# Kernel tuning notes

Hardware: AMD Instinct MI355X
Metric: run time of the kernel (lower is better)

## Reference

```python
import jax, jax.numpy as jnp
import numpy as np

N_USERS = 200000
N_ITEMS = 100000
N_NODES = N_USERS + N_ITEMS
EMBED_DIM = 64
N_LAYERS = 3
N_EDGES = 5000000
BATCH = 4096


def setup_inputs() -> dict:
    key = jax.random.key(0)
    ks = jax.random.split(key, 8)
    # Xavier-uniform-ish init for embedding tables
    lim = float(np.sqrt(6.0 / (N_USERS + EMBED_DIM)))
    user_emb = jax.random.uniform(ks[0], (N_USERS, EMBED_DIM), jnp.float32, -lim, lim)
    lim_i = float(np.sqrt(6.0 / (N_ITEMS + EMBED_DIM)))
    item_emb = jax.random.uniform(ks[1], (N_ITEMS, EMBED_DIM), jnp.float32, -lim_i, lim_i)
    # sparse normalized adjacency in COO form (values ~ 1/sqrt(du*di), use small positives)
    adj_vals = jax.random.uniform(ks[2], (N_EDGES,), jnp.float32, 0.0, 0.1)
    adj_rows = jax.random.randint(ks[3], (N_EDGES,), 0, N_NODES, jnp.int32)
    adj_cols = jax.random.randint(ks[4], (N_EDGES,), 0, N_NODES, jnp.int32)
    users = jax.random.randint(ks[5], (BATCH,), 0, N_USERS, jnp.int32)
    pos_items = jax.random.randint(ks[6], (BATCH,), 0, N_ITEMS, jnp.int32)
    neg_items = jax.random.randint(ks[7], (BATCH,), 0, N_ITEMS, jnp.int32)
    return {
        "user_emb": user_emb, "item_emb": item_emb, "adj_vals": adj_vals,
        "adj_rows": adj_rows, "adj_cols": adj_cols,
        "users": users, "pos_items": pos_items, "neg_items": neg_items,
    }


def _spmm(adj_rows, adj_cols, adj_vals, x):
    # y = A @ x for sparse COO A: gather source rows, scale, scatter-add to dest rows
    msgs = adj_vals[:, None] * x[adj_cols]          # [n_edges, d]
    return jax.ops.segment_sum(msgs, adj_rows, num_segments=N_NODES)


def reference(user_emb, item_emb, adj_vals, adj_rows, adj_cols, users, pos_items, neg_items):
    # E^0 = concat(user, item); E^k = A @ E^{k-1}; final = mean over k=0..K
    E = jnp.concatenate([user_emb, item_emb], axis=0)   # [N_NODES, d]
    acc = E
    cur = E
    for _ in range(N_LAYERS):
        cur = _spmm(adj_rows, adj_cols, adj_vals, cur)
        acc = acc + cur
    E_final = acc / jnp.asarray(N_LAYERS + 1, E.dtype)
    e_u = E_final[users]                         # users index into user block
    e_pos = E_final[N_USERS + pos_items]         # items offset by n_users
    e_neg = E_final[N_USERS + neg_items]
    return jnp.stack([e_u, e_pos, e_neg], axis=0)  # [3, B, d]
```

## Files before the change

kernel.cpp:

```cpp
#include <hip/hip_runtime.h>
#include <hip/hip_fp16.h>
#include <stdint.h>

#define N_USERS   200000
#define N_ITEMS   100000
#define N_NODES   300000
#define EMBED_DIM 64
#define N_EDGES   5000000
#define BATCH     4096

#define ROWS_PER_BUCKET 512
#define PART_K 586
#define PART_B 1024
#define CHUNK  4884
#define PART_L (PART_K * PART_B)
#define SCAN_T 1024
#define SCAN_NB (PART_L / SCAN_T)

#define VAL_SCALE 81920.0f
#define VAL_INV   (1.0f / 81920.0f)
#define FIN_CAP   10240

__device__ __forceinline__ int swz(int b)     { return ((b & 7) << 7) | (b >> 3); }

__global__ void part_count(const int* __restrict__ rows, int* __restrict__ hist) {
    __shared__ int h[PART_K];
    for (int i = threadIdx.x; i < PART_K; i += blockDim.x) h[i] = 0;
    __syncthreads();
    int beg = blockIdx.x * CHUNK;
    int end = min(beg + CHUNK, N_EDGES);
    for (int i = beg + (int)threadIdx.x * 4; i < end; i += blockDim.x * 4) {
        int4 r4 = *(const int4*)(rows + i);
        atomicAdd(&h[r4.x >> 9], 1);
        atomicAdd(&h[r4.y >> 9], 1);
        atomicAdd(&h[r4.z >> 9], 1);
        atomicAdd(&h[r4.w >> 9], 1);
    }
    __syncthreads();
    for (int i = threadIdx.x; i < PART_K; i += blockDim.x)
        hist[blockIdx.x * PART_K + i] = h[i];
}

__global__ void scan_partial(const int* __restrict__ hist,
                             int* __restrict__ local_scan,
                             int* __restrict__ block_sums) {
    __shared__ int sh[SCAN_T];
    int tid = threadIdx.x;
    int gid = blockIdx.x * SCAN_T + tid;
    int p = gid & (PART_B - 1);
    int k = gid >> 10;
    int b = ((p & 127) << 3) | (p >> 7);
    int v = hist[b * PART_K + k];
    sh[tid] = v;
    __syncthreads();
    for (int off = 1; off < SCAN_T; off <<= 1) {
        int t = (tid >= off) ? sh[tid - off] : 0;
        __syncthreads();
        sh[tid] += t;
        __syncthreads();
    }
    local_scan[gid] = sh[tid] - v;
    if (tid == SCAN_T - 1) block_sums[blockIdx.x] = sh[tid];
}

__global__ void scan_addoff(const int* __restrict__ local_scan,
                            const int* __restrict__ block_sums,
                            int* __restrict__ sofs,
                            int* __restrict__ row_ptr) {
    __shared__ int sh[1024];
    int tid = threadIdx.x;
    int v = (tid < SCAN_NB) ? block_sums[tid] : 0;
    sh[tid] = v;
    __syncthreads();
    for (int off = 1; off < 1024; off <<= 1) {
        int t = (tid >= off) ? sh[tid - off] : 0;
        __syncthreads();
        sh[tid] += t;
        __syncthreads();
    }
    int base = (blockIdx.x == 0) ? 0 : sh[blockIdx.x - 1];
    int gid = blockIdx.x * SCAN_T + tid;
    sofs[gid] = local_scan[gid] + base;
    if (gid == 0) row_ptr[N_NODES] = N_EDGES;
}

__global__ void part_scatter(const int* __restrict__ rows,
                             const int* __restrict__ cols,
                             const float* __restrict__ vals,
                             const int* __restrict__ sofs,
                             unsigned int* __restrict__ ppay,
                             unsigned short* __restrict__ prloc) {
    __shared__ int lcnt[PART_K];
    __shared__ int lbase[PART_K];
    __shared__ int gbase[PART_K];
    __shared__ int sc[1024];
    __shared__ unsigned int   pay[CHUNK];
    __shared__ unsigned short rl[CHUNK];
    __shared__ unsigned short bk[CHUNK];
    int b = blockIdx.x;
    int tid = threadIdx.x;
    int myp = swz(b);
    for (int i = tid; i < PART_K; i += 1024) {
        lcnt[i] = 0;
        gbase[i] = sofs[i * PART_B + myp];
    }
    __syncthreads();
    int beg = b * CHUNK;
    int end = min(beg + CHUNK, N_EDGES);
    int n = end - beg;
    for (int i = beg + tid * 4; i < end; i += 4096) {
        int4 r4 = *(const int4*)(rows + i);
        atomicAdd(&lcnt[r4.x >> 9], 1);
        atomicAdd(&lcnt[r4.y >> 9], 1);
        atomicAdd(&lcnt[r4.z >> 9], 1);
        atomicAdd(&lcnt[r4.w >> 9], 1);
    }
    __syncthreads();
    int v = (tid < PART_K) ? lcnt[tid] : 0;
    sc[tid] = v;
    __syncthreads();
    for (int off = 1; off < 1024; off <<= 1) {
        int t = (tid >= off) ? sc[tid - off] : 0;
        __syncthreads();
        sc[tid] += t;
        __syncthreads();
    }
    if (tid < PART_K) {
        int excl = sc[tid] - v;
        lbase[tid] = excl;
        lcnt[tid] = excl;
    }
    __syncthreads();
    for (int i = beg + tid * 4; i < end; i += 4096) {
        int4 r4 = *(const int4*)(rows + i);
        int4 c4 = *(const int4*)(cols + i);
        float4 v4 = *(const float4*)(vals + i);
        int rr[4] = {r4.x, r4.y, r4.z, r4.w};
        int cc[4] = {c4.x, c4.y, c4.z, c4.w};
        float vv[4] = {v4.x, v4.y, v4.z, v4.w};
        #pragma unroll
        for (int j = 0; j < 4; ++j) {
            int r = rr[j];
            int k = r >> 9;
            int p = atomicAdd(&lcnt[k], 1);
            unsigned int q = (unsigned int)min(8191, (int)(vv[j] * VAL_SCALE + 0.5f));
            pay[p] = (unsigned int)cc[j] | (q << 19);
            rl[p] = (unsigned short)(r & 511);
            bk[p] = (unsigned short)k;
        }
    }
    __syncthreads();
    for (int i = tid; i < n; i += 1024) {
        int k = bk[i];
        int a = gbase[k] + (i - lbase[k]);
        ppay[a] = pay[i];
        prloc[a] = rl[i];
    }
}

__global__ void csr_finalize(const unsigned int* __restrict__ ppay,
                             const unsigned short* __restrict__ prloc,
                             const int* __restrict__ sofs,
                             int* __restrict__ row_ptr,
                             unsigned int* __restrict__ sorted) {
    __shared__ int cnt[ROWS_PER_BUCKET];
    __shared__ int cur[ROWS_PER_BUCKET];
    __shared__ int sc[ROWS_PER_BUCKET];
    __shared__ unsigned int obuf[FIN_CAP];
    int k = blockIdx.x;
    int tid = threadIdx.x;
    int seg_beg = sofs[k * PART_B];
    int seg_end = (k + 1 < PART_K) ? sofs[(k + 1) * PART_B] : N_EDGES;
    int n = seg_end - seg_beg;

    cnt[tid] = 0;
    __syncthreads();
    for (int i = seg_beg + tid; i < seg_end; i += ROWS_PER_BUCKET)
        atomicAdd(&cnt[prloc[i]], 1);
    __syncthreads();

    int v = cnt[tid];
    sc[tid] = v;
    __syncthreads();
    for (int off = 1; off < 512; off <<= 1) {
        int t = (tid >= off) ? sc[tid - off] : 0;
        __syncthreads();
        sc[tid] += t;
        __syncthreads();
    }
    int excl = sc[tid] - v;

    int row = k * ROWS_PER_BUCKET + tid;
    if (row < N_NODES) row_ptr[row] = seg_beg + excl;
    cur[tid] = excl;
    __syncthreads();

    if (n <= FIN_CAP) {
        for (int i = seg_beg + tid; i < seg_end; i += ROWS_PER_BUCKET) {
            int r = prloc[i];
            int lp = atomicAdd(&cur[r], 1);
            obuf[lp] = ppay[i];
        }
        __syncthreads();
        for (int i = tid; i < n; i += ROWS_PER_BUCKET)
            sorted[seg_beg + i] = obuf[i];
    } else {
        for (int i = seg_beg + tid; i < seg_end; i += ROWS_PER_BUCKET) {
            int r = prloc[i];
            int lp = atomicAdd(&cur[r], 1);
            sorted[seg_beg + lp] = ppay[i];
        }
    }
}

__global__ void convert_emb(const float* __restrict__ ue,
                            const float* __restrict__ ie,
                            __half* __restrict__ xh) {
    int t = blockIdx.x * blockDim.x + threadIdx.x;
    if (t >= N_NODES * 16) return;
    int flat = t * 4;
    int row = flat >> 6;
    int off = flat & 63;
    const float* src = (row < N_USERS) ? (ue + (size_t)row * 64 + off)
                                       : (ie + (size_t)(row - N_USERS) * 64 + off);
    float4 v = *(const float4*)src;
    __half2 h0 = __floats2half2_rn(v.x, v.y);
    __half2 h1 = __floats2half2_rn(v.z, v.w);
    float2 packed;
    ((__half2*)&packed)[0] = h0;
    ((__half2*)&packed)[1] = h1;
    ((float2*)xh)[t] = packed;
}

#define ACC8(vv, r) { \
    const __half2* hp_ = (const __half2*)&(r); \
    float2 f0_ = __half22float2(hp_[0]); \
    float2 f1_ = __half22float2(hp_[1]); \
    float2 f2_ = __half22float2(hp_[2]); \
    float2 f3_ = __half22float2(hp_[3]); \
    acc[0] += (vv) * f0_.x; acc[1] += (vv) * f0_.y; \
    acc[2] += (vv) * f1_.x; acc[3] += (vv) * f1_.y; \
    acc[4] += (vv) * f2_.x; acc[5] += (vv) * f2_.y; \
    acc[6] += (vv) * f3_.x; acc[7] += (vv) * f3_.y; }

__global__ __launch_bounds__(256, 6)
void spmm_h(const int* __restrict__ row_ptr,
            const unsigned int* __restrict__ sorted,
            const __half* __restrict__ xh,
            __half* __restrict__ yh) {
    int t = blockIdx.x * blockDim.x + threadIdx.x;
    int row = t >> 3;
    int l8 = t & 7;
    if (row >= N_NODES) return;
    const float4* xv = (const float4*)xh;
    int beg = row_ptr[row];
    int end = row_ptr[row + 1];
    float acc[8] = {0.f, 0.f, 0.f, 0.f, 0.f, 0.f, 0.f, 0.f};
    int e = beg;
    for (; e + 8 <= end; e += 8) {
        unsigned int cv[8];
        #pragma unroll
        for (int j = 0; j < 8; ++j) cv[j] = sorted[e + j];
        float4 r[8];
        #pragma unroll
        for (int j = 0; j < 8; ++j)
            r[j] = xv[(size_t)(cv[j] & 0x7FFFF) * 8 + l8];
        #pragma unroll
        for (int j = 0; j < 8; ++j) {
            float v = (float)(cv[j] >> 19) * VAL_INV;
            ACC8(v, r[j]);
        }
    }
    for (; e + 4 <= end; e += 4) {
        unsigned int cv[4];
        #pragma unroll
        for (int j = 0; j < 4; ++j) cv[j] = sorted[e + j];
        float4 r[4];
        #pragma unroll
        for (int j = 0; j < 4; ++j)
            r[j] = xv[(size_t)(cv[j] & 0x7FFFF) * 8 + l8];
        #pragma unroll
        for (int j = 0; j < 4; ++j) {
            float v = (float)(cv[j] >> 19) * VAL_INV;
            ACC8(v, r[j]);
        }
    }
    for (; e < end; ++e) {
        unsigned int cv = sorted[e];
        float4 r0 = xv[(size_t)(cv & 0x7FFFF) * 8 + l8];
        float v = (float)(cv >> 19) * VAL_INV;
        ACC8(v, r0);
    }
    float4 ov;
    ((__half2*)&ov)[0] = __floats2half2_rn(acc[0], acc[1]);
    ((__half2*)&ov)[1] = __floats2half2_rn(acc[2], acc[3]);
    ((__half2*)&ov)[2] = __floats2half2_rn(acc[4], acc[5]);
    ((__half2*)&ov)[3] = __floats2half2_rn(acc[6], acc[7]);
    ((float4*)yh)[(size_t)row * 8 + l8] = ov;
}

__global__ __launch_bounds__(256, 4)
void final_kernel(const int* __restrict__ row_ptr,
                  const unsigned int* __restrict__ sorted,
                  const float* __restrict__ user_emb,
                  const float* __restrict__ item_emb,
                  const __half* __restrict__ E1h,
                  const __half* __restrict__ E2h,
                  const int* __restrict__ users,
                  const int* __restrict__ pos_items,
                  const int* __restrict__ neg_items,
                  float* __restrict__ out) {
    int t = blockIdx.x * blockDim.x + threadIdx.x;
    int slot = t >> 3;
    int l8 = t & 7;
    if (slot >= 3 * BATCH) return;
    int which = slot >> 12;
    int idx   = slot & (BATCH - 1);
    int node;
    if (which == 0)      node = users[idx];
    else if (which == 1) node = N_USERS + pos_items[idx];
    else                 node = N_USERS + neg_items[idx];

    const float4* e2v = (const float4*)E2h;

    float acc[8] = {0.f, 0.f, 0.f, 0.f, 0.f, 0.f, 0.f, 0.f};
    int beg = row_ptr[node];
    int end = row_ptr[node + 1];
    int e = beg;
    for (; e + 8 <= end; e += 8) {
        unsigned int cv[8];
        #pragma unroll
        for (int j = 0; j < 8; ++j) cv[j] = sorted[e + j];
        float4 r[8];
        #pragma unroll
        for (int j = 0; j < 8; ++j)
            r[j] = e2v[(size_t)(cv[j] & 0x7FFFF) * 8 + l8];
        #pragma unroll
        for (int j = 0; j < 8; ++j) {
            float v = (float)(cv[j] >> 19) * VAL_INV;
            ACC8(v, r[j]);
        }
    }
    for (; e + 2 <= end; e += 2) {
        unsigned int cv0 = sorted[e];
        unsigned int cv1 = sorted[e + 1];
        float4 r0 = e2v[(size_t)(cv0 & 0x7FFFF) * 8 + l8];
        float4 r1 = e2v[(size_t)(cv1 & 0x7FFFF) * 8 + l8];
        float v0 = (float)(cv0 >> 19) * VAL_INV;
        float v1 = (float)(cv1 >> 19) * VAL_INV;
        ACC8(v0, r0);
        ACC8(v1, r1);
    }
    if (e < end) {
        unsigned int cv = sorted[e];
        float4 r0 = e2v[(size_t)(cv & 0x7FFFF) * 8 + l8];
        float v = (float)(cv >> 19) * VAL_INV;
        ACC8(v, r0);
    }

    const float* t0 = (node < N_USERS) ? (user_emb + (size_t)node * 64)
                                       : (item_emb + (size_t)(node - N_USERS) * 64);
    float4 e0a = ((const float4*)t0)[l8 * 2];
    float4 e0b = ((const float4*)t0)[l8 * 2 + 1];

    float4 e1c = ((const float4*)E1h)[(size_t)node * 8 + l8];
    float4 e2c = ((const float4*)E2h)[(size_t)node * 8 + l8];
    const __half2* h1 = (const __half2*)&e1c;
    const __half2* h2 = (const __half2*)&e2c;
    float e1[8], e2[8];
    {
        float2 a0 = __half22float2(h1[0]), a1 = __half22float2(h1[1]);
        float2 a2 = __half22float2(h1[2]), a3 = __half22float2(h1[3]);
        e1[0]=a0.x; e1[1]=a0.y; e1[2]=a1.x; e1[3]=a1.y;
        e1[4]=a2.x; e1[5]=a2.y; e1[6]=a3.x; e1[7]=a3.y;
        float2 b0 = __half22float2(h2[0]), b1 = __half22float2(h2[1]);
        float2 b2 = __half22float2(h2[2]), b3 = __half22float2(h2[3]);
        e2[0]=b0.x; e2[1]=b0.y; e2[2]=b1.x; e2[3]=b1.y;
        e2[4]=b2.x; e2[5]=b2.y; e2[6]=b3.x; e2[7]=b3.y;
    }
    float4 ra, rb;
    ra.x = (e0a.x + e1[0] + e2[0] + acc[0]) * 0.25f;
    ra.y = (e0a.y + e1[1] + e2[1] + acc[1]) * 0.25f;
    ra.z = (e0a.z + e1[2] + e2[2] + acc[2]) * 0.25f;
    ra.w = (e0a.w + e1[3] + e2[3] + acc[3]) * 0.25f;
    rb.x = (e0b.x + e1[4] + e2[4] + acc[4]) * 0.25f;
    rb.y = (e0b.y + e1[5] + e2[5] + acc[5]) * 0.25f;
    rb.z = (e0b.z + e1[6] + e2[6] + acc[6]) * 0.25f;
    rb.w = (e0b.w + e1[7] + e2[7] + acc[7]) * 0.25f;
    ((float4*)out)[(size_t)slot * 16 + l8 * 2]     = ra;
    ((float4*)out)[(size_t)slot * 16 + l8 * 2 + 1] = rb;
}

extern "C" void kernel_launch(void* const* d_in, const int* in_sizes, int n_in,
                              void* d_out, int out_size, void* d_ws, size_t ws_size,
                              hipStream_t stream) {
    const float* user_emb  = (const float*)d_in[0];
    const float* item_emb  = (const float*)d_in[1];
    const float* adj_vals  = (const float*)d_in[2];
    const int*   adj_rows  = (const int*)d_in[3];
    const int*   adj_cols  = (const int*)d_in[4];
    const int*   users     = (const int*)d_in[5];
    const int*   pos_items = (const int*)d_in[6];
    const int*   neg_items = (const int*)d_in[7];
    float* out = (float*)d_out;

    char* ws = (char*)d_ws;
    size_t off = 0;
    auto alloc = [&](size_t bytes) -> void* {
        void* p = ws + off;
        off = (off + bytes + 255) & ~(size_t)255;
        return p;
    };
    int*  hist       = (int*) alloc((size_t)(PART_L + 32) * sizeof(int));
    int*  local_scan = (int*) alloc((size_t)(PART_L + 32) * sizeof(int));
    int*  sofs       = (int*) alloc((size_t)(PART_L + 32) * sizeof(int));
    int*  block_sums = (int*) alloc((size_t)(SCAN_NB + 32) * sizeof(int));
    int*  row_ptr    = (int*) alloc((size_t)(N_NODES + 32) * sizeof(int));
    unsigned int*   ppay  = (unsigned int*)  alloc((size_t)N_EDGES * sizeof(unsigned int));
    unsigned short* prloc = (unsigned short*)alloc((size_t)N_EDGES * sizeof(unsigned short));
    unsigned int* sorted = (unsigned int*)alloc((size_t)N_EDGES * sizeof(unsigned int));
    __half* x0h   = (__half*)alloc((size_t)N_NODES * EMBED_DIM * sizeof(__half));
    __half* E1h   = (__half*)alloc((size_t)N_NODES * EMBED_DIM * sizeof(__half));
    __half* E2h   = (__half*)alloc((size_t)N_NODES * EMBED_DIM * sizeof(__half));

    part_count<<<PART_B, 1024, 0, stream>>>(adj_rows, hist);
    scan_partial<<<SCAN_NB, SCAN_T, 0, stream>>>(hist, local_scan, block_sums);
    scan_addoff<<<SCAN_NB, SCAN_T, 0, stream>>>(local_scan, block_sums, sofs, row_ptr);
    part_scatter<<<PART_B, 1024, 0, stream>>>(adj_rows, adj_cols, adj_vals, sofs, ppay, prloc);
    csr_finalize<<<PART_K, ROWS_PER_BUCKET, 0, stream>>>(ppay, prloc, sofs, row_ptr, sorted);

    const int TB = 256;
    convert_emb<<<(N_NODES * 16 + TB - 1) / TB, TB, 0, stream>>>(user_emb, item_emb, x0h);

    int spmm_blocks = (N_NODES * 8 + TB - 1) / TB;
    spmm_h<<<spmm_blocks, TB, 0, stream>>>(row_ptr, sorted, x0h, E1h);
    spmm_h<<<spmm_blocks, TB, 0, stream>>>(row_ptr, sorted, E1h, E2h);

    int final_blocks = (3 * BATCH * 8 + TB - 1) / TB;
    final_kernel<<<final_blocks, TB, 0, stream>>>(
        row_ptr, sorted, user_emb, item_emb, E1h, E2h, users, pos_items, neg_items, out);
}
```

Baseline: 420.4 us.

## Store layer-0 and layer-1 embeddings as scaled FP8 to halve gather traffic

Converts the initial embeddings to scaled FP8 (x1024) and has the first SpMM read and write FP8, while the second SpMM reads FP8 and writes FP16. The goal is to halve the bytes moved by the random row gathers, which dominate the bandwidth-bound SpMM passes. The final kernel no longer reads E1. It recomputes E1 for the batch rows by gathering the FP8 layer-0 table alongside E2 over the same neighbours, then rescales at the end. The cost is lower precision, since FP8 e4m3 has 3 mantissa bits, which risks accuracy tolerance failures.

```diff
diff --git a/kernel.cpp b/kernel.cpp
--- a/kernel.cpp
+++ b/kernel.cpp
@@ -20,6 +20,11 @@
 #define VAL_SCALE 81920.0f
 #define VAL_INV   (1.0f / 81920.0f)
 #define FIN_CAP   10240
+
+#define EMB_SCALE 1024.0f
+#define EMB_INV   (1.0f / 1024.0f)
+
+typedef float f32x2 __attribute__((ext_vector_type(2)));
 
 __device__ __forceinline__ int swz(int b)     { return ((b & 7) << 7) | (b >> 3); }
 
@@ -215,44 +220,53 @@
 
 __global__ void convert_emb(const float* __restrict__ ue,
                             const float* __restrict__ ie,
-                            __half* __restrict__ xh) {
+                            uint2* __restrict__ xf8) {
     int t = blockIdx.x * blockDim.x + threadIdx.x;
-    if (t >= N_NODES * 16) return;
-    int flat = t * 4;
+    if (t >= N_NODES * 8) return;
+    int flat = t * 8;
     int row = flat >> 6;
     int off = flat & 63;
     const float* src = (row < N_USERS) ? (ue + (size_t)row * 64 + off)
                                        : (ie + (size_t)(row - N_USERS) * 64 + off);
-    float4 v = *(const float4*)src;
-    __half2 h0 = __floats2half2_rn(v.x, v.y);
-    __half2 h1 = __floats2half2_rn(v.z, v.w);
-    float2 packed;
-    ((__half2*)&packed)[0] = h0;
-    ((__half2*)&packed)[1] = h1;
-    ((float2*)xh)[t] = packed;
-}
-
-#define ACC8(vv, r) { \
+    float4 a = ((const float4*)src)[0];
+    float4 b = ((const float4*)src)[1];
+    int lo = __builtin_amdgcn_cvt_pk_fp8_f32(a.x * EMB_SCALE, a.y * EMB_SCALE, 0, 0);
+    lo     = __builtin_amdgcn_cvt_pk_fp8_f32(a.z * EMB_SCALE, a.w * EMB_SCALE, lo, 1);
+    int hi = __builtin_amdgcn_cvt_pk_fp8_f32(b.x * EMB_SCALE, b.y * EMB_SCALE, 0, 0);
+    hi     = __builtin_amdgcn_cvt_pk_fp8_f32(b.z * EMB_SCALE, b.w * EMB_SCALE, hi, 1);
+    xf8[t] = make_uint2((unsigned int)lo, (unsigned int)hi);
+}
+
+#define ACCF8A(vv, u, A) { \
+    f32x2 g0_ = __builtin_amdgcn_cvt_pk_f32_fp8((int)(u).x, 0); \
+    f32x2 g1_ = __builtin_amdgcn_cvt_pk_f32_fp8((int)(u).x, 1); \
+    f32x2 g2_ = __builtin_amdgcn_cvt_pk_f32_fp8((int)(u).y, 0); \
+    f32x2 g3_ = __builtin_amdgcn_cvt_pk_f32_fp8((int)(u).y, 1); \
+    A[0] += (vv) * g0_.x; A[1] += (vv) * g0_.y; \
+    A[2] += (vv) * g1_.x; A[3] += (vv) * g1_.y; \
+    A[4] += (vv) * g2_.x; A[5] += (vv) * g2_.y; \
+    A[6] += (vv) * g3_.x; A[7] += (vv) * g3_.y; }
+
+#define ACCHA(vv, r, A) { \
     const __half2* hp_ = (const __half2*)&(r); \
     float2 f0_ = __half22float2(hp_[0]); \
     float2 f1_ = __half22float2(hp_[1]); \
     float2 f2_ = __half22float2(hp_[2]); \
     float2 f3_ = __half22float2(hp_[3]); \
-    acc[0] += (vv) * f0_.x; acc[1] += (vv) * f0_.y; \
-    acc[2] += (vv) * f1_.x; acc[3] += (vv) * f1_.y; \
-    acc[4] += (vv) * f2_.x; acc[5] += (vv) * f2_.y; \
-    acc[6] += (vv) * f3_.x; acc[7] += (vv) * f3_.y; }
+    A[0] += (vv) * f0_.x; A[1] += (vv) * f0_.y; \
+    A[2] += (vv) * f1_.x; A[3] += (vv) * f1_.y; \
+    A[4] += (vv) * f2_.x; A[5] += (vv) * f2_.y; \
+    A[6] += (vv) * f3_.x; A[7] += (vv) * f3_.y; }
 
 __global__ __launch_bounds__(256, 6)
-void spmm_h(const int* __restrict__ row_ptr,
-            const unsigned int* __restrict__ sorted,
-            const __half* __restrict__ xh,
-            __half* __restrict__ yh) {
+void spmm_f8f8(const int* __restrict__ row_ptr,
+               const unsigned int* __restrict__ sorted,
+               const uint2* __restrict__ xf8,
+               uint2* __restrict__ yf8) {
     int t = blockIdx.x * blockDim.x + threadIdx.x;
     int row = t >> 3;
     int l8 = t & 7;
     if (row >= N_NODES) return;
-    const float4* xv = (const float4*)xh;
     int beg = row_ptr[row];
     int end = row_ptr[row + 1];
     float acc[8] = {0.f, 0.f, 0.f, 0.f, 0.f, 0.f, 0.f, 0.f};
@@ -261,35 +275,89 @@
         unsigned int cv[8];
         #pragma unroll
         for (int j = 0; j < 8; ++j) cv[j] = sorted[e + j];
-        float4 r[8];
+        uint2 r[8];
         #pragma unroll
         for (int j = 0; j < 8; ++j)
-            r[j] = xv[(size_t)(cv[j] & 0x7FFFF) * 8 + l8];
+            r[j] = xf8[(size_t)(cv[j] & 0x7FFFF) * 8 + l8];
         #pragma unroll
         for (int j = 0; j < 8; ++j) {
             float v = (float)(cv[j] >> 19) * VAL_INV;
-            ACC8(v, r[j]);
+            ACCF8A(v, r[j], acc);
         }
     }
     for (; e + 4 <= end; e += 4) {
         unsigned int cv[4];
         #pragma unroll
         for (int j = 0; j < 4; ++j) cv[j] = sorted[e + j];
-        float4 r[4];
+        uint2 r[4];
         #pragma unroll
         for (int j = 0; j < 4; ++j)
-            r[j] = xv[(size_t)(cv[j] & 0x7FFFF) * 8 + l8];
+            r[j] = xf8[(size_t)(cv[j] & 0x7FFFF) * 8 + l8];
         #pragma unroll
         for (int j = 0; j < 4; ++j) {
             float v = (float)(cv[j] >> 19) * VAL_INV;
-            ACC8(v, r[j]);
+            ACCF8A(v, r[j], acc);
         }
     }
     for (; e < end; ++e) {
         unsigned int cv = sorted[e];
-        float4 r0 = xv[(size_t)(cv & 0x7FFFF) * 8 + l8];
+        uint2 r0 = xf8[(size_t)(cv & 0x7FFFF) * 8 + l8];
         float v = (float)(cv >> 19) * VAL_INV;
-        ACC8(v, r0);
+        ACCF8A(v, r0, acc);
+    }
+    int lo = __builtin_amdgcn_cvt_pk_fp8_f32(acc[0], acc[1], 0, 0);
+    lo     = __builtin_amdgcn_cvt_pk_fp8_f32(acc[2], acc[3], lo, 1);
+    int hi = __builtin_amdgcn_cvt_pk_fp8_f32(acc[4], acc[5], 0, 0);
+    hi     = __builtin_amdgcn_cvt_pk_fp8_f32(acc[6], acc[7], hi, 1);
+    yf8[(size_t)row * 8 + l8] = make_uint2((unsigned int)lo, (unsigned int)hi);
+}
+
+__global__ __launch_bounds__(256, 6)
+void spmm_f8f16(const int* __restrict__ row_ptr,
+                const unsigned int* __restrict__ sorted,
+                const uint2* __restrict__ xf8,
+                __half* __restrict__ yh) {
+    int t = blockIdx.x * blockDim.x + threadIdx.x;
+    int row = t >> 3;
+    int l8 = t & 7;
+    if (row >= N_NODES) return;
+    int beg = row_ptr[row];
+    int end = row_ptr[row + 1];
+    float acc[8] = {0.f, 0.f, 0.f, 0.f, 0.f, 0.f, 0.f, 0.f};
+    int e = beg;
+    for (; e + 8 <= end; e += 8) {
+        unsigned int cv[8];
+        #pragma unroll
+        for (int j = 0; j < 8; ++j) cv[j] = sorted[e + j];
+        uint2 r[8];
+        #pragma unroll
+        for (int j = 0; j < 8; ++j)
+            r[j] = xf8[(size_t)(cv[j] & 0x7FFFF) * 8 + l8];
+        #pragma unroll
+        for (int j = 0; j < 8; ++j) {
+            float v = (float)(cv[j] >> 19) * VAL_INV;
+            ACCF8A(v, r[j], acc);
+        }
+    }
+    for (; e + 4 <= end; e += 4) {
+        unsigned int cv[4];
+        #pragma unroll
+        for (int j = 0; j < 4; ++j) cv[j] = sorted[e + j];
+        uint2 r[4];
+        #pragma unroll
+        for (int j = 0; j < 4; ++j)
+            r[j] = xf8[(size_t)(cv[j] & 0x7FFFF) * 8 + l8];
+        #pragma unroll
+        for (int j = 0; j < 4; ++j) {
+            float v = (float)(cv[j] >> 19) * VAL_INV;
+            ACCF8A(v, r[j], acc);
+        }
+    }
+    for (; e < end; ++e) {
+        unsigned int cv = sorted[e];
+        uint2 r0 = xf8[(size_t)(cv & 0x7FFFF) * 8 + l8];
+        float v = (float)(cv >> 19) * VAL_INV;
+        ACCF8A(v, r0, acc);
     }
     float4 ov;
     ((__half2*)&ov)[0] = __floats2half2_rn(acc[0], acc[1]);
@@ -304,7 +372,7 @@
                   const unsigned int* __restrict__ sorted,
                   const float* __restrict__ user_emb,
                   const float* __restrict__ item_emb,
-                  const __half* __restrict__ E1h,
+                  const uint2* __restrict__ x0f8,
                   const __half* __restrict__ E2h,
                   const int* __restrict__ users,
                   const int* __restrict__ pos_items,
@@ -323,39 +391,38 @@
 
     const float4* e2v = (const float4*)E2h;
 
-    float acc[8] = {0.f, 0.f, 0.f, 0.f, 0.f, 0.f, 0.f, 0.f};
+    float a1[8] = {0.f, 0.f, 0.f, 0.f, 0.f, 0.f, 0.f, 0.f};
+    float a3[8] = {0.f, 0.f, 0.f, 0.f, 0.f, 0.f, 0.f, 0.f};
     int beg = row_ptr[node];
     int end = row_ptr[node + 1];
     int e = beg;
-    for (; e + 8 <= end; e += 8) {
-        unsigned int cv[8];
-        #pragma unroll
-        for (int j = 0; j < 8; ++j) cv[j] = sorted[e + j];
-        float4 r[8];
-        #pragma unroll
-        for (int j = 0; j < 8; ++j)
-            r[j] = e2v[(size_t)(cv[j] & 0x7FFFF) * 8 + l8];
-        #pragma unroll
-        for (int j = 0; j < 8; ++j) {
+    for (; e + 4 <= end; e += 4) {
+        unsigned int cv[4];
+        #pragma unroll
+        for (int j = 0; j < 4; ++j) cv[j] = sorted[e + j];
+        uint2 rx[4];
+        float4 r2[4];
+        #pragma unroll
+        for (int j = 0; j < 4; ++j) {
+            size_t col = (size_t)(cv[j] & 0x7FFFF);
+            rx[j] = x0f8[col * 8 + l8];
+            r2[j] = e2v[col * 8 + l8];
+        }
+        #pragma unroll
+        for (int j = 0; j < 4; ++j) {
             float v = (float)(cv[j] >> 19) * VAL_INV;
-            ACC8(v, r[j]);
-        }
-    }
-    for (; e + 2 <= end; e += 2) {
-        unsigned int cv0 = sorted[e];
-        unsigned int cv1 = sorted[e + 1];
-        float4 r0 = e2v[(size_t)(cv0 & 0x7FFFF) * 8 + l8];
-        float4 r1 = e2v[(size_t)(cv1 & 0x7FFFF) * 8 + l8];
-        float v0 = (float)(cv0 >> 19) * VAL_INV;
-        float v1 = (float)(cv1 >> 19) * VAL_INV;
-        ACC8(v0, r0);
-        ACC8(v1, r1);
-    }
-    if (e < end) {
+            ACCF8A(v, rx[j], a1);
+            ACCHA(v, r2[j], a3);
+        }
+    }
+    for (; e < end; ++e) {
         unsigned int cv = sorted[e];
-        float4 r0 = e2v[(size_t)(cv & 0x7FFFF) * 8 + l8];
+        size_t col = (size_t)(cv & 0x7FFFF);
+        uint2 rx = x0f8[col * 8 + l8];
+        float4 r2 = e2v[col * 8 + l8];
         float v = (float)(cv >> 19) * VAL_INV;
-        ACC8(v, r0);
+        ACCF8A(v, rx, a1);
+        ACCHA(v, r2, a3);
     }
 
     const float* t0 = (node < N_USERS) ? (user_emb + (size_t)node * 64)
@@ -363,30 +430,24 @@
     float4 e0a = ((const float4*)t0)[l8 * 2];
     float4 e0b = ((const float4*)t0)[l8 * 2 + 1];
 
-    float4 e1c = ((const float4*)E1h)[(size_t)node * 8 + l8];
-    float4 e2c = ((const float4*)E2h)[(size_t)node * 8 + l8];
-    const __half2* h1 = (const __half2*)&e1c;
+    float4 e2c = e2v[(size_t)node * 8 + l8];
     const __half2* h2 = (const __half2*)&e2c;
-    float e1[8], e2[8];
+    float e2[8];
     {
-        float2 a0 = __half22float2(h1[0]), a1 = __half22float2(h1[1]);
-        float2 a2 = __half22float2(h1[2]), a3 = __half22float2(h1[3]);
-        e1[0]=a0.x; e1[1]=a0.y; e1[2]=a1.x; e1[3]=a1.y;
-        e1[4]=a2.x; e1[5]=a2.y; e1[6]=a3.x; e1[7]=a3.y;
         float2 b0 = __half22float2(h2[0]), b1 = __half22float2(h2[1]);
         float2 b2 = __half22float2(h2[2]), b3 = __half22float2(h2[3]);
         e2[0]=b0.x; e2[1]=b0.y; e2[2]=b1.x; e2[3]=b1.y;
         e2[4]=b2.x; e2[5]=b2.y; e2[6]=b3.x; e2[7]=b3.y;
     }
     float4 ra, rb;
-    ra.x = (e0a.x + e1[0] + e2[0] + acc[0]) * 0.25f;
-    ra.y = (e0a.y + e1[1] + e2[1] + acc[1]) * 0.25f;
-    ra.z = (e0a.z + e1[2] + e2[2] + acc[2]) * 0.25f;
-    ra.w = (e0a.w + e1[3] + e2[3] + acc[3]) * 0.25f;
-    rb.x = (e0b.x + e1[4] + e2[4] + acc[4]) * 0.25f;
-    rb.y = (e0b.y + e1[5] + e2[5] + acc[5]) * 0.25f;
-    rb.z = (e0b.z + e1[6] + e2[6] + acc[6]) * 0.25f;
-    rb.w = (e0b.w + e1[7] + e2[7] + acc[7]) * 0.25f;
+    ra.x = (e0a.x + (a1[0] + e2[0] + a3[0]) * EMB_INV) * 0.25f;
+    ra.y = (e0a.y + (a1[1] + e2[1] + a3[1]) * EMB_INV) * 0.25f;
+    ra.z = (e0a.z + (a1[2] + e2[2] + a3[2]) * EMB_INV) * 0.25f;
+    ra.w = (e0a.w + (a1[3] + e2[3] + a3[3]) * EMB_INV) * 0.25f;
+    rb.x = (e0b.x + (a1[4] + e2[4] + a3[4]) * EMB_INV) * 0.25f;
+    rb.y = (e0b.y + (a1[5] + e2[5] + a3[5]) * EMB_INV) * 0.25f;
+    rb.z = (e0b.z + (a1[6] + e2[6] + a3[6]) * EMB_INV) * 0.25f;
+    rb.w = (e0b.w + (a1[7] + e2[7] + a3[7]) * EMB_INV) * 0.25f;
     ((float4*)out)[(size_t)slot * 16 + l8 * 2]     = ra;
     ((float4*)out)[(size_t)slot * 16 + l8 * 2 + 1] = rb;
 }
@@ -419,9 +480,9 @@
     unsigned int*   ppay  = (unsigned int*)  alloc((size_t)N_EDGES * sizeof(unsigned int));
     unsigned short* prloc = (unsigned short*)alloc((size_t)N_EDGES * sizeof(unsigned short));
     unsigned int* sorted = (unsigned int*)alloc((size_t)N_EDGES * sizeof(unsigned int));
-    __half* x0h   = (__half*)alloc((size_t)N_NODES * EMBED_DIM * sizeof(__half));
-    __half* E1h   = (__half*)alloc((size_t)N_NODES * EMBED_DIM * sizeof(__half));
-    __half* E2h   = (__half*)alloc((size_t)N_NODES * EMBED_DIM * sizeof(__half));
+    uint2*  x0f8 = (uint2*) alloc((size_t)N_NODES * EMBED_DIM);
+    uint2*  E1f8 = (uint2*) alloc((size_t)N_NODES * EMBED_DIM);
+    __half* E2h  = (__half*)alloc((size_t)N_NODES * EMBED_DIM * sizeof(__half));
 
     part_count<<<PART_B, 1024, 0, stream>>>(adj_rows, hist);
     scan_partial<<<SCAN_NB, SCAN_T, 0, stream>>>(hist, local_scan, block_sums);
@@ -430,13 +491,13 @@
     csr_finalize<<<PART_K, ROWS_PER_BUCKET, 0, stream>>>(ppay, prloc, sofs, row_ptr, sorted);
 
     const int TB = 256;
-    convert_emb<<<(N_NODES * 16 + TB - 1) / TB, TB, 0, stream>>>(user_emb, item_emb, x0h);
+    convert_emb<<<(N_NODES * 8 + TB - 1) / TB, TB, 0, stream>>>(user_emb, item_emb, x0f8);
 
     int spmm_blocks = (N_NODES * 8 + TB - 1) / TB;
-    spmm_h<<<spmm_blocks, TB, 0, stream>>>(row_ptr, sorted, x0h, E1h);
-    spmm_h<<<spmm_blocks, TB, 0, stream>>>(row_ptr, sorted, E1h, E2h);
+    spmm_f8f8 <<<spmm_blocks, TB, 0, stream>>>(row_ptr, sorted, x0f8, E1f8);
+    spmm_f8f16<<<spmm_blocks, TB, 0, stream>>>(row_ptr, sorted, E1f8, E2h);
 
     int final_blocks = (3 * BATCH * 8 + TB - 1) / TB;
     final_kernel<<<final_blocks, TB, 0, stream>>>(
-        row_ptr, sorted, user_emb, item_emb, E1h, E2h, users, pos_items, neg_items, out);
-}
+        row_ptr, sorted, user_emb, item_emb, x0f8, E2h, users, pos_items, neg_items, out);
+}
```

Result: faster. 394.3 us (-6.2%).
